# Kernel tuning notes

Hardware: AMD Instinct MI355X
Metric: run time of the kernel (lower is better)

Reference implementation:

```python
import jax, jax.numpy as jnp
import numpy as np

B, T, C = 4, 1024, 1024
H = 16
DH = C // H  # 64


def setup_inputs() -> dict:
    key = jax.random.key(0)
    ks = jax.random.split(key, 10)
    s = 0.02
    return {
        "x": jax.random.normal(ks[0], (B, T, C), dtype=jnp.float32),
        "Wq": jax.random.normal(ks[1], (C, C), dtype=jnp.float32) * s,
        "bq": jnp.zeros((C,), dtype=jnp.float32),
        "Wk": jax.random.normal(ks[2], (C, C), dtype=jnp.float32) * s,
        "bk": jnp.zeros((C,), dtype=jnp.float32),
        "Wv": jax.random.normal(ks[3], (C, C), dtype=jnp.float32) * s,
        "bv": jnp.zeros((C,), dtype=jnp.float32),
        "Wp": jax.random.normal(ks[4], (C, C), dtype=jnp.float32) * s,
        "bp": jnp.zeros((C,), dtype=jnp.float32),
    }


def reference(x, Wq, bq, Wk, bk, Wv, bv, Wp, bp):
    b, t, c = x.shape
    # QKV projections, split into heads: [b, H, t, DH]
    def heads(y):
        return y.reshape(b, t, H, DH).transpose(0, 2, 1, 3)
    q = heads(x @ Wq + bq)
    k = heads(x @ Wk + bk)
    v = heads(x @ Wv + bv)
    # Causal attention. Original masks with -inf BEFORE scaling; -inf*scale is
    # still -inf, so mask-then-scale == scale-then-mask.
    scores = jnp.einsum("bhqd,bhkd->bhqk", q, k) * (DH ** -0.5)
    causal = jnp.tril(jnp.ones((t, t), dtype=bool))
    scores = jnp.where(causal, scores, -jnp.inf)
    attn = jax.nn.softmax(scores, axis=-1)  # dropout p=0.0 -> identity
    ctx = jnp.einsum("bhqk,bhkd->bhqd", attn, v)
    ctx = ctx.transpose(0, 2, 1, 3).reshape(b, t, c)
    return ctx @ Wp + bp
```

## Files before the change

kernel.cpp:

```cpp
#include <hip/hip_runtime.h>


typedef unsigned short ushort_t;
typedef __attribute__((ext_vector_type(8))) __bf16 bf16x8;
typedef __attribute__((ext_vector_type(8))) unsigned short us8;
typedef __attribute__((ext_vector_type(4))) unsigned short us4;
typedef __attribute__((ext_vector_type(4))) float f32x4;

#define AS1 __attribute__((address_space(1)))
#define AS3 __attribute__((address_space(3)))

__device__ __forceinline__ ushort_t f2bf(float f) {
  unsigned int u = __float_as_uint(f);
  u += 0x7fffu + ((u >> 16) & 1u);
  return (ushort_t)(u >> 16);
}


__global__ void cvt_x_kernel(const float* __restrict__ x, ushort_t* __restrict__ xb) {
  const int i = blockIdx.x * 256 + threadIdx.x;
  const float4 v = reinterpret_cast<const float4*>(x)[i];
  us4 o;
  o.x = f2bf(v.x); o.y = f2bf(v.y); o.z = f2bf(v.z); o.w = f2bf(v.w);
  reinterpret_cast<us4*>(xb)[i] = o;
}

__global__ void cvt_w4_kernel(const float* __restrict__ Wq, const float* __restrict__ Wk,
                              const float* __restrict__ Wv, const float* __restrict__ Wp,
                              ushort_t* __restrict__ WQKVT, ushort_t* __restrict__ WPT) {
  __shared__ float t[32][33];
  const int z = blockIdx.z;
  const float* W = (z == 0) ? Wq : (z == 1) ? Wk : (z == 2) ? Wv : Wp;
  ushort_t* Wt = (z == 3) ? WPT : (WQKVT + ((size_t)z << 20));
  const float wscale = (z == 0) ? 0.125f : 1.0f;
  const int n0 = blockIdx.x * 32, k0 = blockIdx.y * 32;
  const int tx = threadIdx.x, ty = threadIdx.y;
#pragma unroll
  for (int i = ty; i < 32; i += 8)
    t[i][tx] = W[(size_t)(k0 + i) * 1024 + n0 + tx];
  __syncthreads();
#pragma unroll
  for (int i = ty; i < 32; i += 8)
    Wt[(size_t)(n0 + i) * 1024 + k0 + tx] = f2bf(t[tx][i] * wscale);
}


__global__ __launch_bounds__(512) void gemm_qkv256_kernel(
    const ushort_t* __restrict__ A, const ushort_t* __restrict__ Bt,
    const float* __restrict__ bq, const float* __restrict__ bk,
    const float* __restrict__ bv, ushort_t* __restrict__ QKVB,
    ushort_t* __restrict__ VT) {
  __shared__ ushort_t smem[2][2][256 * 64];
  const int tid = threadIdx.x;
  const int wave = tid >> 6, lane = tid & 63;
  const int lgrp = lane >> 4, lmod = lane & 15;
  const int wr = wave >> 2, wc = wave & 3;
  const int swz = (blockIdx.x & 7) * 24 + (blockIdx.x >> 3);
  const int row0 = (swz / 12) * 256, col0 = (swz % 12) * 256;

  const ushort_t* Ag = A + (size_t)row0 * 1024;
  const ushort_t* Bg = Bt + (size_t)col0 * 1024;

  const int srow = lane >> 3;
  const int sslot = (lane & 7) ^ srow;
  const int xm = lmod & 7;

  auto stage_half = [&](int buf, int t, int h) {
#pragma unroll
    for (int op = 0; op < 2; ++op) {
      const ushort_t* G = (op ? Bg : Ag) + t * 64;
#pragma unroll
      for (int i = 0; i < 2; ++i) {
        const int c0 = h * 1024 + i * 512 + wave * 64;
        __builtin_amdgcn_global_load_lds(
            (AS1 void*)(G + (size_t)((c0 >> 3) + srow) * 1024 + sslot * 8),
            (AS3 void*)((char*)&smem[buf][op][0] + c0 * 16), 16, 0, 0);
      }
    }
  };

  f32x4 acc[8][4] = {};
  constexpr int nt = 16;

  stage_half(0, 0, 0);
  stage_half(0, 0, 1);

  for (int t = 0; t < nt; ++t) {
    const int cur = t & 1, nxt = cur ^ 1;
    const char* cA = (const char*)&smem[cur][0][0];
    const char* cB = (const char*)&smem[cur][1][0];

    if (t + 1 < nt) {
      stage_half(nxt, t + 1, 0);
      asm volatile("s_waitcnt vmcnt(4)" ::: "memory");
    } else {
      asm volatile("s_waitcnt vmcnt(0)" ::: "memory");
    }
    __builtin_amdgcn_sched_barrier(0);
    __builtin_amdgcn_s_barrier();

    bf16x8 b0[4], b1[4], af[4];
#pragma unroll
    for (int ni = 0; ni < 4; ++ni)
      b0[ni] = *reinterpret_cast<const bf16x8*>(
          cB + (wc * 64 + ni * 16 + lmod) * 128 + ((lgrp ^ xm) << 4));
#pragma unroll
    for (int mi = 0; mi < 4; ++mi)
      af[mi] = *reinterpret_cast<const bf16x8*>(
          cA + (wr * 128 + mi * 16 + lmod) * 128 + ((lgrp ^ xm) << 4));
    __builtin_amdgcn_s_setprio(1);
#pragma unroll
    for (int mi = 0; mi < 4; ++mi)
#pragma unroll
      for (int ni = 0; ni < 4; ++ni)
        acc[mi][ni] = __builtin_amdgcn_mfma_f32_16x16x32_bf16(af[mi], b0[ni], acc[mi][ni], 0, 0, 0);
    __builtin_amdgcn_s_setprio(0);
    __builtin_amdgcn_s_barrier();

    if (t + 1 < nt) stage_half(nxt, t + 1, 1);
#pragma unroll
    for (int mi = 0; mi < 4; ++mi)
      af[mi] = *reinterpret_cast<const bf16x8*>(
          cA + (wr * 128 + (4 + mi) * 16 + lmod) * 128 + ((lgrp ^ xm) << 4));
    __builtin_amdgcn_s_setprio(1);
#pragma unroll
    for (int mi = 0; mi < 4; ++mi)
#pragma unroll
      for (int ni = 0; ni < 4; ++ni)
        acc[4 + mi][ni] = __builtin_amdgcn_mfma_f32_16x16x32_bf16(af[mi], b0[ni], acc[4 + mi][ni], 0, 0, 0);
    __builtin_amdgcn_s_setprio(0);
    __builtin_amdgcn_s_barrier();

#pragma unroll
    for (int ni = 0; ni < 4; ++ni)
      b1[ni] = *reinterpret_cast<const bf16x8*>(
          cB + (wc * 64 + ni * 16 + lmod) * 128 + (((4 | lgrp) ^ xm) << 4));
#pragma unroll
    for (int mi = 0; mi < 4; ++mi)
      af[mi] = *reinterpret_cast<const bf16x8*>(
          cA + (wr * 128 + mi * 16 + lmod) * 128 + (((4 | lgrp) ^ xm) << 4));
    __builtin_amdgcn_s_setprio(1);
#pragma unroll
    for (int mi = 0; mi < 4; ++mi)
#pragma unroll
      for (int ni = 0; ni < 4; ++ni)
        acc[mi][ni] = __builtin_amdgcn_mfma_f32_16x16x32_bf16(af[mi], b1[ni], acc[mi][ni], 0, 0, 0);
    __builtin_amdgcn_s_setprio(0);
    __builtin_amdgcn_s_barrier();

#pragma unroll
    for (int mi = 0; mi < 4; ++mi)
      af[mi] = *reinterpret_cast<const bf16x8*>(
          cA + (wr * 128 + (4 + mi) * 16 + lmod) * 128 + (((4 | lgrp) ^ xm) << 4));
    __builtin_amdgcn_s_setprio(1);
#pragma unroll
    for (int mi = 0; mi < 4; ++mi)
#pragma unroll
      for (int ni = 0; ni < 4; ++ni)
        acc[4 + mi][ni] = __builtin_amdgcn_mfma_f32_16x16x32_bf16(af[mi], b1[ni], acc[4 + mi][ni], 0, 0, 0);
    __builtin_amdgcn_s_setprio(0);
    __builtin_amdgcn_s_barrier();
  }

  if (col0 < 2048) {
    const float* bsel = (col0 < 1024) ? bq : bk;
    const float bsc = (col0 < 1024) ? 0.125f : 1.0f;
    float bvv[4];
#pragma unroll
    for (int ni = 0; ni < 4; ++ni)
      bvv[ni] = bsel[(col0 & 1023) + wc * 64 + ni * 16 + lmod] * bsc;
#pragma unroll
    for (int mi = 0; mi < 8; ++mi) {
#pragma unroll
      for (int ni = 0; ni < 4; ++ni) {
        const int col = col0 + wc * 64 + ni * 16 + lmod;
#pragma unroll
        for (int r = 0; r < 4; ++r) {
          const int row = row0 + wr * 128 + mi * 16 + lgrp * 4 + r;
          QKVB[(size_t)row * 3072 + col] = f2bf(acc[mi][ni][r] + bvv[ni]);
        }
      }
    }
  } else {
    float bvv[4];
#pragma unroll
    for (int ni = 0; ni < 4; ++ni)
      bvv[ni] = bv[(col0 - 2048) + wc * 64 + ni * 16 + lmod];
#pragma unroll
    for (int mi = 0; mi < 8; ++mi) {
#pragma unroll
      for (int ni = 0; ni < 4; ++ni) {
        const int hd = (col0 - 2048) + wc * 64 + ni * 16 + lmod;
        const int R = row0 + wr * 128 + mi * 16 + lgrp * 4;
        const int bb = R >> 10, tl = R & 1023;
        us4 o;
#pragma unroll
        for (int r = 0; r < 4; ++r) o[r] = f2bf(acc[mi][ni][r] + bvv[ni]);
        *reinterpret_cast<us4*>(VT + ((size_t)(bb * 16 + (hd >> 6)) * 64 + (hd & 63)) * 1024 + tl) = o;
      }
    }
  }
}


__global__ __launch_bounds__(256, 2) void gemm_proj_kernel(
    const ushort_t* __restrict__ A, const ushort_t* __restrict__ Bt,
    const float* __restrict__ bias, float* __restrict__ Cout) {
  constexpr int BM = 64, WR = 32, MFR = 2, NIT = 3;
  __shared__ ushort_t As[BM * 32];
  __shared__ ushort_t Bs[128 * 32];
  const int tid = threadIdx.x;
  const int wave = tid >> 6, lane = tid & 63;
  const int lgrp = lane >> 4, lmod = lane & 15;
  const int wr = wave >> 1, wc = wave & 1;
  const int cpx = gridDim.x >> 3;
  const int swz = (blockIdx.x & 7) * cpx + (blockIdx.x >> 3);
  const int row0 = (swz / 8) * BM, col0 = (swz % 8) * 128;

  f32x4 acc[MFR][4] = {};

  for (int k0 = 0; k0 < 1024; k0 += 32) {
#pragma unroll
    for (int it = 0; it < NIT; ++it) {
      const int c0 = it * 256 + wave * 64;
      const int c = c0 + lane;
      if (c0 < BM * 4) {
        const int r = c >> 2, kk = (c & 3) << 3;
        __builtin_amdgcn_global_load_lds(
            (AS1 void*)(A + (size_t)(row0 + r) * 1024 + k0 + kk),
            (AS3 void*)(As + (c0 << 3)), 16, 0, 0);
      } else {
        const int cb = c - BM * 4;
        const int r = cb >> 2, kk = (cb & 3) << 3;
        __builtin_amdgcn_global_load_lds(
            (AS1 void*)(Bt + (size_t)(col0 + r) * 1024 + k0 + kk),
            (AS3 void*)(Bs + ((c0 - BM * 4) << 3)), 16, 0, 0);
      }
    }
    __syncthreads();

    bf16x8 af[MFR], bfr[4];
#pragma unroll
    for (int i = 0; i < MFR; ++i)
      af[i] = *reinterpret_cast<const bf16x8*>(&As[(wr * WR + i * 16 + lmod) * 32 + lgrp * 8]);
#pragma unroll
    for (int i = 0; i < 4; ++i)
      bfr[i] = *reinterpret_cast<const bf16x8*>(&Bs[(wc * 64 + i * 16 + lmod) * 32 + lgrp * 8]);
    __builtin_amdgcn_s_setprio(1);
#pragma unroll
    for (int mi = 0; mi < MFR; ++mi)
#pragma unroll
      for (int ni = 0; ni < 4; ++ni)
        acc[mi][ni] = __builtin_amdgcn_mfma_f32_16x16x32_bf16(af[mi], bfr[ni], acc[mi][ni], 0, 0, 0);
    __builtin_amdgcn_s_setprio(0);
    __syncthreads();
  }

  float bvv[4];
#pragma unroll
  for (int ni = 0; ni < 4; ++ni) bvv[ni] = bias[col0 + wc * 64 + ni * 16 + lmod];
#pragma unroll
  for (int mi = 0; mi < MFR; ++mi)
#pragma unroll
    for (int ni = 0; ni < 4; ++ni) {
      const int col = col0 + wc * 64 + ni * 16 + lmod;
#pragma unroll
      for (int r = 0; r < 4; ++r) {
        const int row = row0 + wr * WR + mi * 16 + lgrp * 4 + r;
        Cout[(size_t)row * 1024 + col] = acc[mi][ni][r] + bvv[ni];
      }
    }
}


__global__ __launch_bounds__(256, 2) void attn_kernel(
    const ushort_t* __restrict__ QKV, const ushort_t* __restrict__ VT,
    ushort_t* __restrict__ Og) {
  const int bid = blockIdx.x;
  const int swz = (bid & 7) * 64 + (bid >> 3);
  const int p = swz & 7, bh = swz >> 3;
  const int b = bh >> 4, h = bh & 15;
  const int jmax = 15 - p;
  const int tid = threadIdx.x;
  const int wave = tid >> 6, lane = tid & 63;
  const int lgrp = lane >> 4, lmod = lane & 15;

  __shared__ ushort_t Ks[64 * 72];
  __shared__ ushort_t Vs[64 * 72];
  __shared__ ushort_t Ps[4][16 * 72];

  const size_t xrow0 = (size_t)b * 1024;
  const int qlo = p * 64 + wave * 16;
  const int qhi = jmax * 64 + wave * 16;

  bf16x8 qfl[2], qfh[2];
#pragma unroll
  for (int ks = 0; ks < 2; ++ks) {
    qfl[ks] = *reinterpret_cast<const bf16x8*>(
        QKV + (xrow0 + qlo + lmod) * 3072 + h * 64 + ks * 32 + lgrp * 8);
    qfh[ks] = *reinterpret_cast<const bf16x8*>(
        QKV + (xrow0 + qhi + lmod) * 3072 + h * 64 + ks * 32 + lgrp * 8);
  }

  f32x4 ol[4] = {}, oh[4] = {};
  float ll[4] = {0.f, 0.f, 0.f, 0.f}, lh[4] = {0.f, 0.f, 0.f, 0.f};

  const int sr = tid >> 3;
  const int scc = (tid & 7) << 3;
  us8 kreg0, kreg1, vreg0, vreg1;

  auto load_tile = [&](int j) {
    const ushort_t* kp = QKV + (xrow0 + j * 64 + sr) * 3072 + 1024 + h * 64 + scc;
    kreg0 = *reinterpret_cast<const us8*>(kp);
    kreg1 = *reinterpret_cast<const us8*>(kp + 32 * 3072);
    const ushort_t* vp = VT + ((size_t)bh * 64 + sr) * 1024 + j * 64 + scc;
    vreg0 = *reinterpret_cast<const us8*>(vp);
    vreg1 = *reinterpret_cast<const us8*>(vp + 32 * 1024);
  };
  auto write_tile = [&]() {
    *reinterpret_cast<us8*>(&Ks[sr * 72 + scc]) = kreg0;
    *reinterpret_cast<us8*>(&Ks[(32 + sr) * 72 + scc]) = kreg1;
    *reinterpret_cast<us8*>(&Vs[sr * 72 + scc]) = vreg0;
    *reinterpret_cast<us8*>(&Vs[(32 + sr) * 72 + scc]) = vreg1;
  };

  auto step = [&](const bf16x8* qf, f32x4* oacc, float* lsum, bool diag) {
    f32x4 s[4];
    __builtin_amdgcn_s_setprio(1);
#pragma unroll
    for (int cg = 0; cg < 4; ++cg) {
      f32x4 a = {};
#pragma unroll
      for (int ks = 0; ks < 2; ++ks) {
        bf16x8 kf = *reinterpret_cast<const bf16x8*>(
            &Ks[(cg * 16 + lmod) * 72 + ks * 32 + lgrp * 8]);
        a = __builtin_amdgcn_mfma_f32_16x16x32_bf16(qf[ks], kf, a, 0, 0, 0);
      }
      s[cg] = a;
    }
    __builtin_amdgcn_s_setprio(0);
    if (diag) {
      const int qloc = wave * 16 + lgrp * 4;
#pragma unroll
      for (int cg = 0; cg < 4; ++cg) {
        const int kcol = cg * 16 + lmod;
#pragma unroll
        for (int r = 0; r < 4; ++r)
          if (kcol > qloc + r) s[cg][r] = -1e30f;
      }
    }
#pragma unroll
    for (int cg = 0; cg < 4; ++cg)
#pragma unroll
      for (int r = 0; r < 4; ++r) s[cg][r] = __expf(s[cg][r]);
#pragma unroll
    for (int r = 0; r < 4; ++r)
      lsum[r] += (s[0][r] + s[1][r]) + (s[2][r] + s[3][r]);
#pragma unroll
    for (int cg = 0; cg < 4; ++cg)
#pragma unroll
      for (int r = 0; r < 4; ++r)
        Ps[wave][(lgrp * 4 + r) * 72 + cg * 16 + lmod] = f2bf(s[cg][r]);
    __builtin_amdgcn_s_setprio(1);
#pragma unroll
    for (int ks = 0; ks < 2; ++ks) {
      bf16x8 pf = *reinterpret_cast<const bf16x8*>(
          &Ps[wave][lmod * 72 + ks * 32 + lgrp * 8]);
#pragma unroll
      for (int dhg = 0; dhg < 4; ++dhg) {
        bf16x8 vf = *reinterpret_cast<const bf16x8*>(
            &Vs[(dhg * 16 + lmod) * 72 + ks * 32 + lgrp * 8]);
        oacc[dhg] = __builtin_amdgcn_mfma_f32_16x16x32_bf16(pf, vf, oacc[dhg], 0, 0, 0);
      }
    }
    __builtin_amdgcn_s_setprio(0);
  };

  load_tile(0);
  for (int j = 0; j <= jmax; ++j) {
    __syncthreads();
    write_tile();
    __syncthreads();
    if (j < jmax) load_tile(j + 1);
    if (j <= p) step(qfl, ol, ll, j == p);
    step(qfh, oh, lh, j == jmax);
  }

#pragma unroll
  for (int m = 1; m <= 8; m <<= 1)
#pragma unroll
    for (int r = 0; r < 4; ++r) {
      ll[r] += __shfl_xor(ll[r], m);
      lh[r] += __shfl_xor(lh[r], m);
    }

#pragma unroll
  for (int dhg = 0; dhg < 4; ++dhg) {
    const int col = h * 64 + dhg * 16 + lmod;
#pragma unroll
    for (int r = 0; r < 4; ++r) {
      Og[(xrow0 + qlo + lgrp * 4 + r) * 1024 + col] = f2bf(ol[dhg][r] / ll[r]);
      Og[(xrow0 + qhi + lgrp * 4 + r) * 1024 + col] = f2bf(oh[dhg][r] / lh[r]);
    }
  }
}


extern "C" void kernel_launch(void* const* d_in, const int* in_sizes, int n_in,
                              void* d_out, int out_size, void* d_ws, size_t ws_size,
                              hipStream_t stream) {
  const float* x  = (const float*)d_in[0];
  const float* Wq = (const float*)d_in[1];
  const float* bq = (const float*)d_in[2];
  const float* Wk = (const float*)d_in[3];
  const float* bk = (const float*)d_in[4];
  const float* Wv = (const float*)d_in[5];
  const float* bv = (const float*)d_in[6];
  const float* Wp = (const float*)d_in[7];
  const float* bp = (const float*)d_in[8];
  float* out = (float*)d_out;

  char* ws = (char*)d_ws;
  ushort_t* XB    = (ushort_t*)(ws);
  ushort_t* WQKVT = (ushort_t*)(ws + ( 8ull << 20));
  ushort_t* WPT   = (ushort_t*)(ws + (14ull << 20));
  ushort_t* QKVB  = (ushort_t*)(ws + (16ull << 20));
  ushort_t* VT    = (ushort_t*)(ws + (40ull << 20));

  cvt_x_kernel<<<4096, 256, 0, stream>>>(x, XB);
  cvt_w4_kernel<<<dim3(32, 32, 4), dim3(32, 8), 0, stream>>>(Wq, Wk, Wv, Wp, WQKVT, WPT);
  gemm_qkv256_kernel<<<192, 512, 0, stream>>>(XB, WQKVT, bq, bk, bv, QKVB, VT);
  attn_kernel<<<512, 256, 0, stream>>>(QKVB, VT, XB);
  gemm_proj_kernel<<<512, 256, 0, stream>>>(XB, WPT, bp, out);
}
```

Baseline: 96.09 us.

## Batch all A-fragment LDS reads per k-half and drop intermediate barriers

The GEMM main loop now loads all eight A fragments for each k-half from LDS at once, instead of reloading them in groups of four between MFMA batches. The three intra-iteration workgroup barriers are removed, leaving one barrier per tile. The second-half global staging is moved so it is issued after the first-half MFMAs. This aims to cut barrier stalls and interleave LDS reads with MFMA work more freely. In exchange it needs more VGPRs for the larger fragment arrays, which could cost occupancy or cause spills, and it gives up the lockstep wave scheduling the barriers enforced.

```diff
diff --git a/kernel.cpp b/kernel.cpp
--- a/kernel.cpp
+++ b/kernel.cpp
@@ -99,66 +99,51 @@
     __builtin_amdgcn_sched_barrier(0);
     __builtin_amdgcn_s_barrier();
 
-    bf16x8 b0[4], b1[4], af[4];
+    bf16x8 a0[8], b0[4], a1[8], b1[4];
 #pragma unroll
     for (int ni = 0; ni < 4; ++ni)
       b0[ni] = *reinterpret_cast<const bf16x8*>(
           cB + (wc * 64 + ni * 16 + lmod) * 128 + ((lgrp ^ xm) << 4));
 #pragma unroll
+    for (int mi = 0; mi < 8; ++mi)
+      a0[mi] = *reinterpret_cast<const bf16x8*>(
+          cA + (wr * 128 + mi * 16 + lmod) * 128 + ((lgrp ^ xm) << 4));
+
+    __builtin_amdgcn_s_setprio(1);
+#pragma unroll
     for (int mi = 0; mi < 4; ++mi)
-      af[mi] = *reinterpret_cast<const bf16x8*>(
-          cA + (wr * 128 + mi * 16 + lmod) * 128 + ((lgrp ^ xm) << 4));
-    __builtin_amdgcn_s_setprio(1);
-#pragma unroll
-    for (int mi = 0; mi < 4; ++mi)
 #pragma unroll
       for (int ni = 0; ni < 4; ++ni)
-        acc[mi][ni] = __builtin_amdgcn_mfma_f32_16x16x32_bf16(af[mi], b0[ni], acc[mi][ni], 0, 0, 0);
-    __builtin_amdgcn_s_setprio(0);
-    __builtin_amdgcn_s_barrier();
-
-    if (t + 1 < nt) stage_half(nxt, t + 1, 1);
-#pragma unroll
-    for (int mi = 0; mi < 4; ++mi)
-      af[mi] = *reinterpret_cast<const bf16x8*>(
-          cA + (wr * 128 + (4 + mi) * 16 + lmod) * 128 + ((lgrp ^ xm) << 4));
-    __builtin_amdgcn_s_setprio(1);
-#pragma unroll
-    for (int mi = 0; mi < 4; ++mi)
-#pragma unroll
-      for (int ni = 0; ni < 4; ++ni)
-        acc[4 + mi][ni] = __builtin_amdgcn_mfma_f32_16x16x32_bf16(af[mi], b0[ni], acc[4 + mi][ni], 0, 0, 0);
-    __builtin_amdgcn_s_setprio(0);
-    __builtin_amdgcn_s_barrier();
+        acc[mi][ni] = __builtin_amdgcn_mfma_f32_16x16x32_bf16(a0[mi], b0[ni], acc[mi][ni], 0, 0, 0);
+    __builtin_amdgcn_s_setprio(0);
 
 #pragma unroll
     for (int ni = 0; ni < 4; ++ni)
       b1[ni] = *reinterpret_cast<const bf16x8*>(
           cB + (wc * 64 + ni * 16 + lmod) * 128 + (((4 | lgrp) ^ xm) << 4));
 #pragma unroll
+    for (int mi = 0; mi < 8; ++mi)
+      a1[mi] = *reinterpret_cast<const bf16x8*>(
+          cA + (wr * 128 + mi * 16 + lmod) * 128 + (((4 | lgrp) ^ xm) << 4));
+
+    __builtin_amdgcn_s_setprio(1);
+#pragma unroll
     for (int mi = 0; mi < 4; ++mi)
-      af[mi] = *reinterpret_cast<const bf16x8*>(
-          cA + (wr * 128 + mi * 16 + lmod) * 128 + (((4 | lgrp) ^ xm) << 4));
-    __builtin_amdgcn_s_setprio(1);
-#pragma unroll
-    for (int mi = 0; mi < 4; ++mi)
 #pragma unroll
       for (int ni = 0; ni < 4; ++ni)
-        acc[mi][ni] = __builtin_amdgcn_mfma_f32_16x16x32_bf16(af[mi], b1[ni], acc[mi][ni], 0, 0, 0);
-    __builtin_amdgcn_s_setprio(0);
-    __builtin_amdgcn_s_barrier();
-
-#pragma unroll
-    for (int mi = 0; mi < 4; ++mi)
-      af[mi] = *reinterpret_cast<const bf16x8*>(
-          cA + (wr * 128 + (4 + mi) * 16 + lmod) * 128 + (((4 | lgrp) ^ xm) << 4));
-    __builtin_amdgcn_s_setprio(1);
-#pragma unroll
-    for (int mi = 0; mi < 4; ++mi)
+        acc[4 + mi][ni] = __builtin_amdgcn_mfma_f32_16x16x32_bf16(a0[4 + mi], b0[ni], acc[4 + mi][ni], 0, 0, 0);
+    __builtin_amdgcn_s_setprio(0);
+
+    if (t + 1 < nt) stage_half(nxt, t + 1, 1);
+
+    __builtin_amdgcn_s_setprio(1);
+#pragma unroll
+    for (int mi = 0; mi < 8; ++mi)
 #pragma unroll
       for (int ni = 0; ni < 4; ++ni)
-        acc[4 + mi][ni] = __builtin_amdgcn_mfma_f32_16x16x32_bf16(af[mi], b1[ni], acc[4 + mi][ni], 0, 0, 0);
-    __builtin_amdgcn_s_setprio(0);
+        acc[mi][ni] = __builtin_amdgcn_mfma_f32_16x16x32_bf16(a1[mi], b1[ni], acc[mi][ni], 0, 0, 0);
+    __builtin_amdgcn_s_setprio(0);
+
     __builtin_amdgcn_s_barrier();
   }
 
```

Result: faster. 93.84 us (-2.3%).
